# Performance work log

Measured on AMD Instinct MI355X. Metric: run time of the kernel, lower is better.

## Reference

```python
import jax, jax.numpy as jnp
import numpy as np

IN_F = 256
OUT_F = 256
ALPHA = 0.2  # leaky-relu slope
NEG_INF = -9e15


def setup_inputs() -> dict:
    key = jax.random.key(0)
    ks = jax.random.split(key, 8)
    N_e, N_kc = 10000, 2000
    exercise_h = jax.random.normal(ks[0], (N_e, IN_F), dtype=jnp.float32)
    kc_h = jax.random.normal(ks[1], (N_kc, IN_F), dtype=jnp.float32)
    adj = jax.random.randint(ks[2], (N_e, N_kc), 0, 2, dtype=jnp.int32)
    # parameters (kaiming-ish scaling)
    W1 = jax.random.normal(ks[3], (IN_F, OUT_F), dtype=jnp.float32) * np.sqrt(2.0 / IN_F)
    E = jax.random.normal(ks[4], (IN_F, OUT_F), dtype=jnp.float32) * np.sqrt(2.0 / IN_F)
    a = jax.random.normal(ks[5], (2 * OUT_F, 1), dtype=jnp.float32) * np.sqrt(2.0 / (2 * OUT_F))
    rd_w = jax.random.normal(ks[6], (OUT_F, 2 * OUT_F), dtype=jnp.float32) * np.sqrt(2.0 / (2 * OUT_F))
    rd_b = jnp.zeros((OUT_F,), dtype=jnp.float32)
    return {"exercise_h": exercise_h, "kc_h": kc_h, "adj": adj,
            "W1": W1, "E": E, "a": a, "rd_w": rd_w, "rd_b": rd_b}


def reference(exercise_h, kc_h, adj, W1, E, a, rd_w, rd_b):
    kc_Wh = kc_h @ W1            # [N_kc, D]
    ex_Wh = exercise_h @ W1      # [N_e, D]
    # a . concat(ex_Wh_i, kc_Wh_j) == a1.ex_Wh_i + a2.kc_Wh_j  (avoids [N_e,N_kc,2D] tensor)
    a1 = a[:OUT_F, 0]
    a2 = a[OUT_F:, 0]
    e = jax.nn.leaky_relu((ex_Wh @ a1)[:, None] + (kc_Wh @ a2)[None, :], negative_slope=ALPHA)  # [N_e, N_kc]
    logits = jnp.where(adj > 0, e, jnp.float32(NEG_INF))
    attention = jax.nn.softmax(logits, axis=1)
    new_kc = attention @ kc_Wh           # [N_e, D]
    ex_Eh = exercise_h @ E               # [N_e, D]
    feat = jnp.concatenate([new_kc, new_kc * ex_Eh], axis=1)  # [N_e, 2D]
    out = feat @ rd_w.T + rd_b
    return jax.nn.elu(out)
```

## Files before the change

kernel.cpp:

```cpp
#include <hip/hip_runtime.h>

#define N_E 10000
#define N_KC 2000
#define ALPHA 0.2f

typedef __attribute__((ext_vector_type(8))) short short8;
typedef __attribute__((ext_vector_type(4))) float f32x4;

__device__ float g_w1a1[256];
__device__ float g_t[2048];
__device__ __align__(16) unsigned short g_W1T_pk[16 * 8 * 512];
__device__ __align__(16) unsigned short g_ET_pk[16 * 8 * 512];
__device__ __align__(16) unsigned short g_rdw_pk[16 * 16 * 512];
__device__ __align__(16) unsigned short g_kcWh_pk[16 * 64 * 512];

__device__ __forceinline__ unsigned short f2bf(float f) {
  union { float f; unsigned int u; } v; v.f = f;
  unsigned int r = v.u + 0x7FFFu + ((v.u >> 16) & 1u);
  return (unsigned short)(r >> 16);
}

__device__ __forceinline__ void cvt_store4(float4 v, unsigned short* dst) {
  ushort4 o;
  o.x = f2bf(v.x); o.y = f2bf(v.y); o.z = f2bf(v.z); o.w = f2bf(v.w);
  *reinterpret_cast<ushort4*>(dst) = o;
}

__global__ __launch_bounds__(256) void prep_kernel(
    const float* __restrict__ W1, const float* __restrict__ E,
    const float* __restrict__ a, const float* __restrict__ rd_w) {
  int b = blockIdx.x, tid = threadIdx.x;
  if (b < 32) {
#pragma unroll
    for (int s2 = 0; s2 < 2; ++s2) {
      int sId = b * 512 + tid + s2 * 256;
      int ct = sId >> 10, rem = sId & 1023;
      int kt = rem >> 6, lane = rem & 63;
      int g = lane >> 4, r = lane & 15;
      const float* src = rd_w + (size_t)(ct * 16 + r) * 512 + kt * 32 + g * 8;
      unsigned short* dst = g_rdw_pk + (size_t)sId * 8;
      cvt_store4(*(const float4*)src, dst);
      cvt_store4(*(const float4*)(src + 4), dst + 4);
    }
  } else if (b < 48) {
#pragma unroll
    for (int s2 = 0; s2 < 2; ++s2) {
      int sId = (b - 32) * 512 + tid + s2 * 256;
      int ct = sId >> 9, rem = sId & 511;
      int kt = rem >> 6, lane = rem & 63;
      int g = lane >> 4, r = lane & 15;
      int col = ct * 16 + r, k = kt * 32 + g * 8;
      unsigned short* dst = g_W1T_pk + (size_t)sId * 8;
      ushort4 o0, o1;
      o0.x = f2bf(W1[(k + 0) * 256 + col]); o0.y = f2bf(W1[(k + 1) * 256 + col]);
      o0.z = f2bf(W1[(k + 2) * 256 + col]); o0.w = f2bf(W1[(k + 3) * 256 + col]);
      o1.x = f2bf(W1[(k + 4) * 256 + col]); o1.y = f2bf(W1[(k + 5) * 256 + col]);
      o1.z = f2bf(W1[(k + 6) * 256 + col]); o1.w = f2bf(W1[(k + 7) * 256 + col]);
      *(ushort4*)dst = o0; *(ushort4*)(dst + 4) = o1;
    }
  } else if (b < 64) {
#pragma unroll
    for (int s2 = 0; s2 < 2; ++s2) {
      int sId = (b - 48) * 512 + tid + s2 * 256;
      int ct = sId >> 9, rem = sId & 511;
      int kt = rem >> 6, lane = rem & 63;
      int g = lane >> 4, r = lane & 15;
      int col = ct * 16 + r, k = kt * 32 + g * 8;
      unsigned short* dst = g_ET_pk + (size_t)sId * 8;
      ushort4 o0, o1;
      o0.x = f2bf(E[(k + 0) * 256 + col]); o0.y = f2bf(E[(k + 1) * 256 + col]);
      o0.z = f2bf(E[(k + 2) * 256 + col]); o0.w = f2bf(E[(k + 3) * 256 + col]);
      o1.x = f2bf(E[(k + 4) * 256 + col]); o1.y = f2bf(E[(k + 5) * 256 + col]);
      o1.z = f2bf(E[(k + 6) * 256 + col]); o1.w = f2bf(E[(k + 7) * 256 + col]);
      *(ushort4*)dst = o0; *(ushort4*)(dst + 4) = o1;
    }
  } else if (b == 64) {
    float acc = 0.f;
    for (int q = 0; q < 64; ++q) {
      float4 wv = *(const float4*)(W1 + (size_t)tid * 256 + q * 4);
      float4 a4 = *(const float4*)(a + q * 4);
      acc += wv.x * a4.x + wv.y * a4.y + wv.z * a4.z + wv.w * a4.w;
    }
    g_w1a1[tid] = acc;
  } else {
    for (int idx = tid; idx < 16 * 2 * 512; idx += 256) {
      int ct = idx >> 10, rem = idx & 1023;
      int kt = 62 + (rem >> 9), off = rem & 511;
      g_kcWh_pk[((size_t)ct * 64 + kt) * 512 + off] = 0;
    }
    if (tid < 48) g_t[2000 + tid] = 0.f;
  }
}

__global__ __launch_bounds__(256) void kc_mfma_kernel(
    const float* __restrict__ kc_h, const float* __restrict__ a) {
  __shared__ float tred[4][4][4];
  int tid = threadIdx.x, lane = tid & 63, w = tid >> 6;
  int r = lane & 15, g = lane >> 4;
  int j0 = blockIdx.x * 16;
  f32x4 acc[4] = {{0.f,0.f,0.f,0.f},{0.f,0.f,0.f,0.f},
                  {0.f,0.f,0.f,0.f},{0.f,0.f,0.f,0.f}};
  for (int kk = 0; kk < 8; ++kk) {
    int k = kk * 32 + g * 8;
    const float* src = kc_h + (size_t)(j0 + r) * 256 + k;
    float4 x0 = *(const float4*)src, x1 = *(const float4*)(src + 4);
    short8 af = {(short)f2bf(x0.x), (short)f2bf(x0.y), (short)f2bf(x0.z),
                 (short)f2bf(x0.w), (short)f2bf(x1.x), (short)f2bf(x1.y),
                 (short)f2bf(x1.z), (short)f2bf(x1.w)};
#pragma unroll
    for (int n = 0; n < 4; ++n) {
      short8 bf = *(const short8*)(g_W1T_pk + ((size_t)(w * 4 + n) * 8 + kk) *
                                                  512 + lane * 8);
      acc[n] = __builtin_amdgcn_mfma_f32_16x16x32_bf16(af, bf, acc[n], 0, 0, 0);
    }
  }
  int j = j0 + g * 4;
  int kt = j >> 5, lsub = ((j >> 3) & 3) * 16 + r, sub = (g & 1) * 4;
#pragma unroll
  for (int n = 0; n < 4; ++n) {
    int ct = w * 4 + n;
    ushort4 o;
    o.x = f2bf(acc[n][0]); o.y = f2bf(acc[n][1]);
    o.z = f2bf(acc[n][2]); o.w = f2bf(acc[n][3]);
    *reinterpret_cast<ushort4*>(
        g_kcWh_pk + ((size_t)ct * 64 + kt) * 512 + lsub * 8 + sub) = o;
  }
  float a2v[4];
#pragma unroll
  for (int n = 0; n < 4; ++n) a2v[n] = a[256 + w * 64 + n * 16 + r];
  float tp[4];
#pragma unroll
  for (int q = 0; q < 4; ++q)
    tp[q] = acc[0][q] * a2v[0] + acc[1][q] * a2v[1] + acc[2][q] * a2v[2] +
            acc[3][q] * a2v[3];
#pragma unroll
  for (int off = 1; off < 16; off <<= 1)
#pragma unroll
    for (int q = 0; q < 4; ++q) tp[q] += __shfl_xor(tp[q], off, 64);
  if (r == 0)
#pragma unroll
    for (int q = 0; q < 4; ++q) tred[w][g][q] = tp[q];
  __syncthreads();
  if (tid < 16)
    g_t[j0 + tid] = tred[0][tid >> 2][tid & 3] + tred[1][tid >> 2][tid & 3] +
                    tred[2][tid >> 2][tid & 3] + tred[3][tid >> 2][tid & 3];
}

#define FST 536
__global__ __launch_bounds__(512, 2) void main_kernel(
    const float* __restrict__ exh, const int* __restrict__ adj,
    const float* __restrict__ rd_b, float* __restrict__ out) {
  __shared__ __align__(16) unsigned char smem[64512 + 8192];
  __shared__ float sv_s[16];
  __shared__ float inv_s[16];
  unsigned short* P_lds = (unsigned short*)smem;
  float* t_s = (float*)(smem + 64512);
  unsigned short* feat_s = (unsigned short*)smem;

  int tid = threadIdx.x, w = tid >> 6, lane = tid & 63;
  int i0 = blockIdx.x * 16;

  ((float4*)t_s)[tid] = ((const float4*)g_t)[tid];
  {
    int row = tid >> 5, seg = tid & 31;
    const float* xsrc = exh + (size_t)(i0 + row) * 256 + seg * 8;
    float4 x0 = *(const float4*)xsrc, x1 = *(const float4*)(xsrc + 4);
    const float* wsrc = g_w1a1 + seg * 8;
    float4 w0 = *(const float4*)wsrc, w1 = *(const float4*)(wsrc + 4);
    float sp = x0.x * w0.x + x0.y * w0.y + x0.z * w0.z + x0.w * w0.w +
               x1.x * w1.x + x1.y * w1.y + x1.z * w1.z + x1.w * w1.w;
    sp += __shfl_xor(sp, 1, 64);
    sp += __shfl_xor(sp, 2, 64);
    sp += __shfl_xor(sp, 4, 64);
    sp += __shfl_xor(sp, 8, 64);
    sp += __shfl_xor(sp, 16, 64);
    if ((tid & 31) == 0) sv_s[row] = sp;
  }
  __syncthreads();

  {
    int kks = lane >> 2, g = lane & 3;
    float dsum[2] = {0.f, 0.f};
#pragma unroll
    for (int rr = 0; rr < 2; ++rr) {
      int row = w * 2 + rr;
      float svr = sv_s[row];
      const int* arow = adj + (size_t)(i0 + row) * N_KC;
#pragma unroll
      for (int v = 0; v < 4; ++v) {
        int kk = v * 16 + kks;
        int c0 = kk * 32 + g * 8;
        int4 a0v = {0, 0, 0, 0}, a1v = {0, 0, 0, 0};
        if (c0 + 4 <= N_KC) a0v = *(const int4*)(arow + c0);
        if (c0 + 8 <= N_KC) a1v = *(const int4*)(arow + c0 + 4);
        float4 t0 = *(const float4*)(t_s + c0);
        float4 t1 = *(const float4*)(t_s + c0 + 4);
        float tv[8] = {t0.x, t0.y, t0.z, t0.w, t1.x, t1.y, t1.z, t1.w};
        int av[8] = {a0v.x, a0v.y, a0v.z, a0v.w, a1v.x, a1v.y, a1v.z, a1v.w};
        unsigned ub[8];
#pragma unroll
        for (int j = 0; j < 8; ++j) {
          float x = svr + tv[j];
          float lx = fmaxf(x, ALPHA * x);
          float pv = (av[j] > 0) ? __expf(lx) : 0.f;
          dsum[rr] += pv;
          ub[j] = __float_as_uint(pv) + 0x8000u;
        }
        int4 pk;
        pk.x = (int)((ub[0] >> 16) | (ub[1] & 0xFFFF0000u));
        pk.y = (int)((ub[2] >> 16) | (ub[3] & 0xFFFF0000u));
        pk.z = (int)((ub[4] >> 16) | (ub[5] & 0xFFFF0000u));
        pk.w = (int)((ub[6] >> 16) | (ub[7] & 0xFFFF0000u));
        if (kk < 63) {
          int slot = (row ^ kks) | (g << 4);
          *(int4*)(P_lds + ((size_t)kk << 9) + (slot << 3)) = pk;
        }
      }
    }
#pragma unroll
    for (int rr = 0; rr < 2; ++rr) {
      float d = dsum[rr];
      d += __shfl_xor(d, 1, 64);
      d += __shfl_xor(d, 2, 64);
      d += __shfl_xor(d, 4, 64);
      d += __shfl_xor(d, 8, 64);
      d += __shfl_xor(d, 16, 64);
      d += __shfl_xor(d, 32, 64);
      if (lane == 0) inv_s[w * 2 + rr] = 1.f / fmaxf(d, 1e-30f);
    }
  }
  __syncthreads();

  f32x4 accP[2][2] = {{{0.f,0.f,0.f,0.f},{0.f,0.f,0.f,0.f}},
                      {{0.f,0.f,0.f,0.f},{0.f,0.f,0.f,0.f}}};
  const unsigned short* bb0 =
      g_kcWh_pk + (size_t)(w * 2 + 0) * 64 * 512 + lane * 8;
  const unsigned short* bb1 =
      g_kcWh_pk + (size_t)(w * 2 + 1) * 64 * 512 + lane * 8;
#pragma unroll 7
  for (int kk = 0; kk < 63; ++kk) {
    short8 a = *(const short8*)(P_lds + ((size_t)kk << 9) +
                                ((lane ^ (kk & 15)) << 3));
    short8 b0 = *(const short8*)(bb0 + ((size_t)kk << 9));
    short8 b1 = *(const short8*)(bb1 + ((size_t)kk << 9));
    accP[0][kk & 1] = __builtin_amdgcn_mfma_f32_16x16x32_bf16(a, b0, accP[0][kk & 1], 0, 0, 0);
    accP[1][kk & 1] = __builtin_amdgcn_mfma_f32_16x16x32_bf16(a, b1, accP[1][kk & 1], 0, 0, 0);
  }

  int r2 = lane & 15, g2 = lane >> 4;
  f32x4 accE[2] = {{0.f,0.f,0.f,0.f},{0.f,0.f,0.f,0.f}};
#pragma unroll
  for (int kk8 = 0; kk8 < 8; ++kk8) {
    const float* xs = exh + (size_t)(i0 + r2) * 256 + kk8 * 32 + g2 * 8;
    float4 x0 = *(const float4*)xs, x1 = *(const float4*)(xs + 4);
    short8 a0 = {(short)f2bf(x0.x), (short)f2bf(x0.y), (short)f2bf(x0.z),
                 (short)f2bf(x0.w), (short)f2bf(x1.x), (short)f2bf(x1.y),
                 (short)f2bf(x1.z), (short)f2bf(x1.w)};
#pragma unroll
    for (int n = 0; n < 2; ++n) {
      short8 bf = *(const short8*)(g_ET_pk + ((size_t)(w * 2 + n) * 8 + kk8) *
                                                 512 + lane * 8);
      accE[n] = __builtin_amdgcn_mfma_f32_16x16x32_bf16(a0, bf, accE[n], 0, 0, 0);
    }
  }
  __syncthreads();

#pragma unroll
  for (int n = 0; n < 2; ++n) {
    int col = w * 32 + n * 16 + r2;
#pragma unroll
    for (int q = 0; q < 4; ++q) {
      int row = g2 * 4 + q;
      float nk = (accP[n][0][q] + accP[n][1][q]) * inv_s[row];
      feat_s[(size_t)row * FST + col] = f2bf(nk);
      feat_s[(size_t)row * FST + 256 + col] = f2bf(nk * accE[n][q]);
    }
  }
  __syncthreads();

  f32x4 accO[2] = {{0.f,0.f,0.f,0.f},{0.f,0.f,0.f,0.f}};
#pragma unroll
  for (int kt = 0; kt < 16; ++kt) {
    int k = kt * 32 + g2 * 8;
    short8 a0 = *(const short8*)(feat_s + (size_t)r2 * FST + k);
#pragma unroll
    for (int n = 0; n < 2; ++n) {
      short8 bf = *(const short8*)(g_rdw_pk + ((size_t)(w * 2 + n) * 16 + kt) *
                                                  512 + lane * 8);
      accO[n] = __builtin_amdgcn_mfma_f32_16x16x32_bf16(a0, bf, accO[n], 0, 0, 0);
    }
  }
#pragma unroll
  for (int n = 0; n < 2; ++n) {
    int col = w * 32 + n * 16 + r2;
    float bias = rd_b[col];
#pragma unroll
    for (int q = 0; q < 4; ++q) {
      int row = i0 + g2 * 4 + q;
      float x = accO[n][q] + bias;
      float res = x > 0.f ? x : (__expf(x) - 1.f);
      out[(size_t)row * 256 + col] = res;
    }
  }
}

extern "C" void kernel_launch(void* const* d_in, const int* in_sizes, int n_in,
                              void* d_out, int out_size, void* d_ws,
                              size_t ws_size, hipStream_t stream) {
  const float* exh  = (const float*)d_in[0];
  const float* kc_h = (const float*)d_in[1];
  const int*   adj  = (const int*)d_in[2];
  const float* W1   = (const float*)d_in[3];
  const float* E    = (const float*)d_in[4];
  const float* a    = (const float*)d_in[5];
  const float* rd_w = (const float*)d_in[6];
  const float* rd_b = (const float*)d_in[7];
  float* out = (float*)d_out;

  prep_kernel<<<66, 256, 0, stream>>>(W1, E, a, rd_w);
  kc_mfma_kernel<<<N_KC / 16, 256, 0, stream>>>(kc_h, a);
  main_kernel<<<N_E / 16, 512, 0, stream>>>(exh, adj, rd_b, out);
}
```

Measured before the change: 218.4 us.

## Split main kernel across 16 waves with one column tile per wave

Doubles the main kernel block to 1024 threads so each wave owns one 16-column tile of the attention, E and output GEMMs instead of two. The P-tile build is remapped so each wave covers four k-steps across all 16 rows, with an unswizzled LDS layout. Row sums are combined with LDS atomics. The exercise rows are converted to bf16 once and staged in LDS for the E GEMM rather than reloaded from global memory. Work per wave drops, but the aggressive launch bounds may force a low register cap and spilling, and the unswizzled P writes may bank-conflict.

```diff
diff --git a/kernel.cpp b/kernel.cpp
--- a/kernel.cpp
+++ b/kernel.cpp
@@ -147,48 +147,49 @@
 }
 
 #define FST 536
-__global__ __launch_bounds__(512, 2) void main_kernel(
+__global__ __launch_bounds__(1024, 8) void main_kernel(
     const float* __restrict__ exh, const int* __restrict__ adj,
     const float* __restrict__ rd_b, float* __restrict__ out) {
-  __shared__ __align__(16) unsigned char smem[64512 + 8192];
-  __shared__ float sv_s[16];
-  __shared__ float inv_s[16];
+  __shared__ __align__(16) unsigned char smem[80960];
   unsigned short* P_lds = (unsigned short*)smem;
-  float* t_s = (float*)(smem + 64512);
   unsigned short* feat_s = (unsigned short*)smem;
+  float* denom_s = (float*)(smem + 64512);
+  float* inv_s = (float*)(smem + 64576);
+  float* sv_s = (float*)(smem + 64640);
+  float* t_s = (float*)(smem + 64704);
+  unsigned short* exh_pk_s = (unsigned short*)(smem + 72768);
 
   int tid = threadIdx.x, w = tid >> 6, lane = tid & 63;
+  int r = lane & 15, g = lane >> 4;
   int i0 = blockIdx.x * 16;
 
-  ((float4*)t_s)[tid] = ((const float4*)g_t)[tid];
-  {
-    int row = tid >> 5, seg = tid & 31;
-    const float* xsrc = exh + (size_t)(i0 + row) * 256 + seg * 8;
-    float4 x0 = *(const float4*)xsrc, x1 = *(const float4*)(xsrc + 4);
-    const float* wsrc = g_w1a1 + seg * 8;
-    float4 w0 = *(const float4*)wsrc, w1 = *(const float4*)(wsrc + 4);
-    float sp = x0.x * w0.x + x0.y * w0.y + x0.z * w0.z + x0.w * w0.w +
-               x1.x * w1.x + x1.y * w1.y + x1.z * w1.z + x1.w * w1.w;
-    sp += __shfl_xor(sp, 1, 64);
-    sp += __shfl_xor(sp, 2, 64);
-    sp += __shfl_xor(sp, 4, 64);
-    sp += __shfl_xor(sp, 8, 64);
-    sp += __shfl_xor(sp, 16, 64);
-    if ((tid & 31) == 0) sv_s[row] = sp;
-  }
-  __syncthreads();
-
-  {
-    int kks = lane >> 2, g = lane & 3;
-    float dsum[2] = {0.f, 0.f};
-#pragma unroll
-    for (int rr = 0; rr < 2; ++rr) {
-      int row = w * 2 + rr;
-      float svr = sv_s[row];
-      const int* arow = adj + (size_t)(i0 + row) * N_KC;
-#pragma unroll
-      for (int v = 0; v < 4; ++v) {
-        int kk = v * 16 + kks;
+  if (tid < 1008) ((float2*)t_s)[tid] = ((const float2*)g_t)[tid];
+  if (tid < 16) denom_s[tid] = 0.f;
+  {
+    const float* xsrc = exh + (size_t)(i0 + w) * 256 + lane * 4;
+    float4 x = *(const float4*)xsrc;
+    const float* wsrc = g_w1a1 + lane * 4;
+    float4 wv = *(const float4*)wsrc;
+    float sp = x.x * wv.x + x.y * wv.y + x.z * wv.z + x.w * wv.w;
+#pragma unroll
+    for (int off = 1; off < 64; off <<= 1) sp += __shfl_xor(sp, off, 64);
+    if (lane == 0) sv_s[w] = sp;
+    ushort4 o;
+    o.x = f2bf(x.x); o.y = f2bf(x.y); o.z = f2bf(x.z); o.w = f2bf(x.w);
+    int c = lane * 4;
+    int kk8 = c >> 5, gf = (c >> 3) & 3, hh = (c >> 2) & 1;
+    *(ushort4*)(exh_pk_s + kk8 * 512 + (w + 16 * gf) * 8 + hh * 4) = o;
+  }
+  __syncthreads();
+
+  {
+    float svr = sv_s[r];
+    const int* arow = adj + (size_t)(i0 + r) * N_KC;
+    float dsum = 0.f;
+#pragma unroll 2
+    for (int v = 0; v < 4; ++v) {
+      int kk = w * 4 + v;
+      if (kk < 63) {
         int c0 = kk * 32 + g * 8;
         int4 a0v = {0, 0, 0, 0}, a1v = {0, 0, 0, 0};
         if (c0 + 4 <= N_KC) a0v = *(const int4*)(arow + c0);
@@ -203,7 +204,7 @@
           float x = svr + tv[j];
           float lx = fmaxf(x, ALPHA * x);
           float pv = (av[j] > 0) ? __expf(lx) : 0.f;
-          dsum[rr] += pv;
+          dsum += pv;
           ub[j] = __float_as_uint(pv) + 0x8000u;
         }
         int4 pk;
@@ -211,95 +212,65 @@
         pk.y = (int)((ub[2] >> 16) | (ub[3] & 0xFFFF0000u));
         pk.z = (int)((ub[4] >> 16) | (ub[5] & 0xFFFF0000u));
         pk.w = (int)((ub[6] >> 16) | (ub[7] & 0xFFFF0000u));
-        if (kk < 63) {
-          int slot = (row ^ kks) | (g << 4);
-          *(int4*)(P_lds + ((size_t)kk << 9) + (slot << 3)) = pk;
-        }
+        *(int4*)(P_lds + (size_t)kk * 512 + lane * 8) = pk;
       }
     }
-#pragma unroll
-    for (int rr = 0; rr < 2; ++rr) {
-      float d = dsum[rr];
-      d += __shfl_xor(d, 1, 64);
-      d += __shfl_xor(d, 2, 64);
-      d += __shfl_xor(d, 4, 64);
-      d += __shfl_xor(d, 8, 64);
-      d += __shfl_xor(d, 16, 64);
-      d += __shfl_xor(d, 32, 64);
-      if (lane == 0) inv_s[w * 2 + rr] = 1.f / fmaxf(d, 1e-30f);
-    }
-  }
-  __syncthreads();
-
-  f32x4 accP[2][2] = {{{0.f,0.f,0.f,0.f},{0.f,0.f,0.f,0.f}},
-                      {{0.f,0.f,0.f,0.f},{0.f,0.f,0.f,0.f}}};
-  const unsigned short* bb0 =
-      g_kcWh_pk + (size_t)(w * 2 + 0) * 64 * 512 + lane * 8;
-  const unsigned short* bb1 =
-      g_kcWh_pk + (size_t)(w * 2 + 1) * 64 * 512 + lane * 8;
-#pragma unroll 7
+    dsum += __shfl_xor(dsum, 16, 64);
+    dsum += __shfl_xor(dsum, 32, 64);
+    if (lane < 16) atomicAdd(&denom_s[lane], dsum);
+  }
+  __syncthreads();
+  if (tid < 16) inv_s[tid] = 1.f / fmaxf(denom_s[tid], 1e-30f);
+
+  f32x4 accP[2] = {{0.f,0.f,0.f,0.f},{0.f,0.f,0.f,0.f}};
+  const unsigned short* bb = g_kcWh_pk + (size_t)w * 64 * 512 + lane * 8;
+#pragma unroll 4
   for (int kk = 0; kk < 63; ++kk) {
-    short8 a = *(const short8*)(P_lds + ((size_t)kk << 9) +
-                                ((lane ^ (kk & 15)) << 3));
-    short8 b0 = *(const short8*)(bb0 + ((size_t)kk << 9));
-    short8 b1 = *(const short8*)(bb1 + ((size_t)kk << 9));
-    accP[0][kk & 1] = __builtin_amdgcn_mfma_f32_16x16x32_bf16(a, b0, accP[0][kk & 1], 0, 0, 0);
-    accP[1][kk & 1] = __builtin_amdgcn_mfma_f32_16x16x32_bf16(a, b1, accP[1][kk & 1], 0, 0, 0);
-  }
-
-  int r2 = lane & 15, g2 = lane >> 4;
-  f32x4 accE[2] = {{0.f,0.f,0.f,0.f},{0.f,0.f,0.f,0.f}};
+    short8 a = *(const short8*)(P_lds + (size_t)kk * 512 + lane * 8);
+    short8 b = *(const short8*)(bb + (size_t)kk * 512);
+    accP[kk & 1] =
+        __builtin_amdgcn_mfma_f32_16x16x32_bf16(a, b, accP[kk & 1], 0, 0, 0);
+  }
+
+  f32x4 accE = {0.f, 0.f, 0.f, 0.f};
 #pragma unroll
   for (int kk8 = 0; kk8 < 8; ++kk8) {
-    const float* xs = exh + (size_t)(i0 + r2) * 256 + kk8 * 32 + g2 * 8;
-    float4 x0 = *(const float4*)xs, x1 = *(const float4*)(xs + 4);
-    short8 a0 = {(short)f2bf(x0.x), (short)f2bf(x0.y), (short)f2bf(x0.z),
-                 (short)f2bf(x0.w), (short)f2bf(x1.x), (short)f2bf(x1.y),
-                 (short)f2bf(x1.z), (short)f2bf(x1.w)};
-#pragma unroll
-    for (int n = 0; n < 2; ++n) {
-      short8 bf = *(const short8*)(g_ET_pk + ((size_t)(w * 2 + n) * 8 + kk8) *
-                                                 512 + lane * 8);
-      accE[n] = __builtin_amdgcn_mfma_f32_16x16x32_bf16(a0, bf, accE[n], 0, 0, 0);
-    }
-  }
-  __syncthreads();
-
-#pragma unroll
-  for (int n = 0; n < 2; ++n) {
-    int col = w * 32 + n * 16 + r2;
+    short8 a0 = *(const short8*)(exh_pk_s + kk8 * 512 + lane * 8);
+    short8 bf =
+        *(const short8*)(g_ET_pk + ((size_t)(w * 8 + kk8)) * 512 + lane * 8);
+    accE = __builtin_amdgcn_mfma_f32_16x16x32_bf16(a0, bf, accE, 0, 0, 0);
+  }
+  __syncthreads();
+
+  {
+    int col = w * 16 + r;
 #pragma unroll
     for (int q = 0; q < 4; ++q) {
-      int row = g2 * 4 + q;
-      float nk = (accP[n][0][q] + accP[n][1][q]) * inv_s[row];
+      int row = g * 4 + q;
+      float nk = (accP[0][q] + accP[1][q]) * inv_s[row];
       feat_s[(size_t)row * FST + col] = f2bf(nk);
-      feat_s[(size_t)row * FST + 256 + col] = f2bf(nk * accE[n][q]);
-    }
-  }
-  __syncthreads();
-
-  f32x4 accO[2] = {{0.f,0.f,0.f,0.f},{0.f,0.f,0.f,0.f}};
+      feat_s[(size_t)row * FST + 256 + col] = f2bf(nk * accE[q]);
+    }
+  }
+  __syncthreads();
+
+  f32x4 accO = {0.f, 0.f, 0.f, 0.f};
 #pragma unroll
   for (int kt = 0; kt < 16; ++kt) {
-    int k = kt * 32 + g2 * 8;
-    short8 a0 = *(const short8*)(feat_s + (size_t)r2 * FST + k);
-#pragma unroll
-    for (int n = 0; n < 2; ++n) {
-      short8 bf = *(const short8*)(g_rdw_pk + ((size_t)(w * 2 + n) * 16 + kt) *
-                                                  512 + lane * 8);
-      accO[n] = __builtin_amdgcn_mfma_f32_16x16x32_bf16(a0, bf, accO[n], 0, 0, 0);
-    }
-  }
-#pragma unroll
-  for (int n = 0; n < 2; ++n) {
-    int col = w * 32 + n * 16 + r2;
+    int k = kt * 32 + g * 8;
+    short8 a0 = *(const short8*)(feat_s + (size_t)r * FST + k);
+    short8 bf =
+        *(const short8*)(g_rdw_pk + ((size_t)(w * 16 + kt)) * 512 + lane * 8);
+    accO = __builtin_amdgcn_mfma_f32_16x16x32_bf16(a0, bf, accO, 0, 0, 0);
+  }
+  {
+    int col = w * 16 + r;
     float bias = rd_b[col];
 #pragma unroll
     for (int q = 0; q < 4; ++q) {
-      int row = i0 + g2 * 4 + q;
-      float x = accO[n][q] + bias;
-      float res = x > 0.f ? x : (__expf(x) - 1.f);
-      out[(size_t)row * 256 + col] = res;
+      int row = i0 + g * 4 + q;
+      float x = accO[q] + bias;
+      out[(size_t)row * 256 + col] = x > 0.f ? x : (__expf(x) - 1.f);
     }
   }
 }
@@ -319,5 +290,5 @@
 
   prep_kernel<<<66, 256, 0, stream>>>(W1, E, a, rd_w);
   kc_mfma_kernel<<<N_KC / 16, 256, 0, stream>>>(kc_h, a);
-  main_kernel<<<N_E / 16, 512, 0, stream>>>(exh, adj, rd_b, out);
-}
+  main_kernel<<<N_E / 16, 1024, 0, stream>>>(exh, adj, rd_b, out);
+}
```

After: 194.3 us. 1.12x faster.
